# Kernel optimization log

Measured on AMD Instinct MI355X. Metric: run time of the kernel, lower is better.

## Reference

```python
import jax, jax.numpy as jnp
import numpy as np

B, T, C, H = 2, 2048, 1024, 16
HD = C // H  # head dim = 64


def setup_inputs() -> dict:
    key = jax.random.key(0)
    ks = jax.random.split(key, 5)
    s = 1.0 / np.sqrt(C)
    return {
        "x": jax.random.normal(ks[0], (B, T, C), dtype=jnp.float32),
        "W_attn": jax.random.normal(ks[1], (3 * C, C), dtype=jnp.float32) * s,
        "b_attn": jax.random.normal(ks[2], (3 * C,), dtype=jnp.float32) * 0.02,
        "W_proj": jax.random.normal(ks[3], (C, C), dtype=jnp.float32) * s,
        "b_proj": jax.random.normal(ks[4], (C,), dtype=jnp.float32) * 0.02,
    }


def reference(x, W_attn, b_attn, W_proj, b_proj):
    Bx, Tx, Cx = x.shape
    # fused QKV projection (torch Linear: x @ W.T + b)
    qkv = x @ W_attn.T + b_attn                      # [B,T,3C]
    q, k, v = jnp.split(qkv, 3, axis=-1)
    # [B,T,C] -> [B,H,T,hd]
    q = q.reshape(Bx, Tx, H, HD).transpose(0, 2, 1, 3)
    k = k.reshape(Bx, Tx, H, HD).transpose(0, 2, 1, 3)
    v = v.reshape(Bx, Tx, H, HD).transpose(0, 2, 1, 3)
    scale = 1.0 / np.sqrt(HD)
    att = jnp.einsum('bhqd,bhkd->bhqk', q, k) * scale  # [B,H,T,T]
    causal = jnp.tril(jnp.ones((Tx, Tx), dtype=bool))
    att = jnp.where(causal[None, None], att, -jnp.inf)
    att = jax.nn.softmax(att, axis=-1)
    y = jnp.einsum('bhqk,bhkd->bhqd', att, v)          # [B,H,T,hd]
    y = y.transpose(0, 2, 1, 3).reshape(Bx, Tx, Cx)
    return y @ W_proj.T + b_proj
```

## Files before the change

kernel.cpp:

```cpp
#include <hip/hip_runtime.h>

typedef unsigned short ushort_t;
typedef __bf16 bf16x8 __attribute__((ext_vector_type(8)));
typedef float f32x4 __attribute__((ext_vector_type(4)));
typedef unsigned u32x4 __attribute__((ext_vector_type(4)));

__device__ inline ushort_t f2bf(float f) {
  unsigned int u = __builtin_bit_cast(unsigned int, f);
  u += 0x7fff + ((u >> 16) & 1);
  return (ushort_t)(u >> 16);
}

__device__ inline unsigned pk_bf(float a, float b) {
  unsigned r;
  asm("v_cvt_pk_bf16_f32 %0, %1, %2" : "=v"(r) : "v"(a), "v"(b));
  return r;
}

__device__ inline void async_ld16(const ushort_t* g, const ushort_t* l) {
  __builtin_amdgcn_global_load_lds(
      (const __attribute__((address_space(1))) void*)g,
      (__attribute__((address_space(3))) void*)l, 16, 0, 0);
}

template <int IMM>
__device__ inline void waitcnt_barrier() {
  asm volatile("" ::: "memory");
  __builtin_amdgcn_s_waitcnt(IMM);
  __builtin_amdgcn_s_barrier();
  asm volatile("" ::: "memory");
}

__global__ void cvt_all(const float* __restrict__ x, const float* __restrict__ wa,
                        const float* __restrict__ wp, ushort_t* __restrict__ xb,
                        ushort_t* __restrict__ wab, ushort_t* __restrict__ wpb) {
  int i = blockIdx.x * 256 + threadIdx.x;
  const float* src;
  ushort_t* dst;
  int off;
  if (i < 1048576) { src = x; dst = xb; off = i; }
  else if (i < 1835008) { src = wa; dst = wab; off = i - 1048576; }
  else { src = wp; dst = wpb; off = i - 1835008; }
  float4 f = ((const float4*)src)[off];
  unsigned long long p = (unsigned long long)f2bf(f.x)
      | ((unsigned long long)f2bf(f.y) << 16)
      | ((unsigned long long)f2bf(f.z) << 32)
      | ((unsigned long long)f2bf(f.w) << 48);
  ((unsigned long long*)dst)[off] = p;
}

template <int BM, int BN, int IM, int JN, int MODE, int TPB>
__global__ __launch_bounds__(TPB) void gemm_bt(
    const ushort_t* __restrict__ A, const ushort_t* __restrict__ B,
    const float* __restrict__ bias, float* __restrict__ Cf,
    ushort_t* __restrict__ Cb, ushort_t* __restrict__ vtb,
    int M, int N, int K, int ldc, float qscale) {
  constexpr int NWN = BN / (JN * 16);
  constexpr int NL = (BM + BN) * 32 / (TPB * 8);
  constexpr int WIMM = 0x0F70 | NL;
  __shared__ __align__(16) ushort_t As[3][BM * 32];
  __shared__ __align__(16) ushort_t Bs[3][BN * 32];
  const int tid = threadIdx.x;
  const int wave = tid >> 6, lane = tid & 63;
  const int quad = lane >> 4, l16 = lane & 15;
  const int wr = wave / NWN, wc = wave % NWN;
  const int wm = wr * IM * 16, wn = wc * JN * 16;
  const int m0 = blockIdx.y * BM, n0 = blockIdx.x * BN;
  const ushort_t* Ag = A + (size_t)m0 * K;
  const ushort_t* Bg = B + (size_t)n0 * K;
  const int slot = (quad ^ ((l16 >> 1) & 3)) * 8;
  f32x4 acc[IM][JN] = {};

  auto stage = [&](int kt, int bsel) {
    int k0 = kt * 32;
#pragma unroll
    for (int p = 0; p < BM * 4 / TPB; ++p) {
      int ci = p * TPB + tid;
      int row = ci >> 2, ch = (ci & 3) ^ ((ci >> 3) & 3);
      async_ld16(Ag + (size_t)row * K + k0 + ch * 8, As[bsel] + (p * TPB + wave * 64) * 8);
    }
#pragma unroll
    for (int p = 0; p < BN * 4 / TPB; ++p) {
      int ci = p * TPB + tid;
      int row = ci >> 2, ch = (ci & 3) ^ ((ci >> 3) & 3);
      async_ld16(Bg + (size_t)row * K + k0 + ch * 8, Bs[bsel] + (p * TPB + wave * 64) * 8);
    }
  };

  const int KT = K / 32;
  stage(0, 0);
  stage(1, 1);
  for (int kt = 0; kt < KT; ++kt) {
    waitcnt_barrier<WIMM>();
    if (kt + 2 < KT) stage(kt + 2, (kt + 2) % 3);
    const ushort_t* Ac = As[kt % 3];
    const ushort_t* Bc = Bs[kt % 3];
    bf16x8 af[IM], bfr[JN];
#pragma unroll
    for (int i = 0; i < IM; ++i)
      af[i] = *(const bf16x8*)(Ac + (wm + i * 16 + l16) * 32 + slot);
#pragma unroll
    for (int j = 0; j < JN; ++j)
      bfr[j] = *(const bf16x8*)(Bc + (wn + j * 16 + l16) * 32 + slot);
#pragma unroll
    for (int i = 0; i < IM; ++i)
#pragma unroll
      for (int j = 0; j < JN; ++j)
        acc[i][j] = __builtin_amdgcn_mfma_f32_16x16x32_bf16(af[i], bfr[j], acc[i][j], 0, 0, 0);
  }

  if (MODE == 1 && n0 >= 2048) {
#pragma unroll
    for (int j = 0; j < JN; ++j) {
      int col = n0 + wn + j * 16 + l16;
      int cv = col - 2048;
      float bv = bias[col];
      size_t rowbase = ((size_t)(cv >> 6)) * 64 + (cv & 63);
#pragma unroll
      for (int i = 0; i < IM; ++i) {
        int rowb = m0 + wm + i * 16 + quad * 4;
        int bb = rowb >> 11, t = rowb & 2047;
        uint2 pp;
        pp.x = pk_bf(acc[i][j][0] + bv, acc[i][j][1] + bv);
        pp.y = pk_bf(acc[i][j][2] + bv, acc[i][j][3] + bv);
        *(uint2*)(vtb + (((size_t)bb * 1024 + rowbase) * 2048 + t)) = pp;
      }
    }
    return;
  }
#pragma unroll
  for (int j = 0; j < JN; ++j) {
    int col = n0 + wn + j * 16 + l16;
    float bv = bias[col];
    float sc = (MODE == 1 && col < 1024) ? qscale : 1.0f;
#pragma unroll
    for (int i = 0; i < IM; ++i)
#pragma unroll
      for (int r = 0; r < 4; ++r) {
        int row = m0 + wm + i * 16 + quad * 4 + r;
        float v = (acc[i][j][r] + bv) * sc;
        if (MODE == 1)
          Cb[(size_t)row * ldc + col] = f2bf(v);
        else
          Cf[(size_t)row * ldc + col] = v;
      }
  }
}

__global__ __launch_bounds__(256, 2) void flash7(
    const ushort_t* __restrict__ qk, const ushort_t* __restrict__ vt,
    ushort_t* __restrict__ y) {
  __shared__ __align__(16) ushort_t Kb[3][4096];
  __shared__ __align__(16) ushort_t Vb[3][4096];
  const int tid = threadIdx.x, wave = tid >> 6, lane = tid & 63;
  const int quad = lane >> 4, l16 = lane & 15;
  const int r7 = l16 & 7;
  const int fK = (l16 & 3) | (((l16 >> 2) & 1) << 2);
  const int kbase = (16 * (l16 >> 2) + (l16 & 3)) * 64;
  const int xx = blockIdx.x, bh = blockIdx.y;
  const int Q = (bh < 16) ? (15 - xx) : xx;
  const int b = bh >> 4, h = bh & 15;
  const int bT = b * 2048;
  const int qw = Q * 128 + wave * 32;

  bf16x8 qf[2][2];
#pragma unroll
  for (int f = 0; f < 2; ++f) {
    const ushort_t* qrow = qk + (size_t)(bT + qw + f * 16 + l16) * 2048 + h * 64 + quad * 8;
    qf[f][0] = *(const bf16x8*)(qrow);
    qf[f][1] = *(const bf16x8*)(qrow + 32);
  }

  auto stage = [&](int kt, int bsel) {
    int k0 = kt * 64;
#pragma unroll
    for (int i = 0; i < 2; ++i) {
      int ci = i * 256 + tid;
      int row = ci >> 3;
      int chk = (ci & 7) ^ ((row & 3) | (((row >> 4) & 1) << 2));
      int chv = (ci & 7) ^ (row & 7);
      async_ld16(qk + (size_t)(bT + k0 + row) * 2048 + 1024 + h * 64 + chk * 8,
                 Kb[bsel] + (i * 256 + wave * 64) * 8);
      async_ld16(vt + (size_t)(bh * 64 + row) * 2048 + k0 + chv * 8,
                 Vb[bsel] + (i * 256 + wave * 64) * 8);
    }
  };

  f32x4 o[4][2] = {};
  float lac[2] = {0.f, 0.f};
  const int KT = 2 * Q + 2;

  stage(0, 0);
  stage(1, 1);
  for (int kt = 0; kt < KT; ++kt) {
    const int cur = kt % 3;
    if (kt + 1 < KT) waitcnt_barrier<0x0F74>();
    else             waitcnt_barrier<0x0F70>();
    if (kt + 2 < KT) stage(kt + 2, (kt + 2) % 3);
    const ushort_t* Kc = Kb[cur];
    const ushort_t* Vc = Vb[cur];
    bf16x8 kf[4][2];
#pragma unroll
    for (int j = 0; j < 4; ++j)
#pragma unroll
      for (int ks = 0; ks < 2; ++ks)
        kf[j][ks] = *(const bf16x8*)(Kc + kbase + j * 256 + (((ks * 4 + quad) ^ fK) * 8));
    f32x4 s[4][2] = {};
#pragma unroll
    for (int ks = 0; ks < 2; ++ks)
#pragma unroll
      for (int j = 0; j < 4; ++j) {
        s[j][0] = __builtin_amdgcn_mfma_f32_16x16x32_bf16(kf[j][ks], qf[0][ks], s[j][0], 0, 0, 0);
        s[j][1] = __builtin_amdgcn_mfma_f32_16x16x32_bf16(kf[j][ks], qf[1][ks], s[j][1], 0, 0, 0);
      }
    if (kt >= KT - 2) {
#pragma unroll
      for (int f = 0; f < 2; ++f) {
        int qloc = qw + f * 16 + l16;
#pragma unroll
        for (int j = 0; j < 4; ++j)
#pragma unroll
          for (int r = 0; r < 4; ++r)
            if (kt * 64 + quad * 16 + j * 4 + r > qloc) s[j][f][r] = -1e30f;
      }
    }
#pragma unroll
    for (int f = 0; f < 2; ++f)
#pragma unroll
      for (int j = 0; j < 4; ++j)
#pragma unroll
        for (int r = 0; r < 4; ++r) {
          float pv = exp2f(s[j][f][r]);
          s[j][f][r] = pv;
          lac[f] += pv;
        }
    bf16x8 pf[2][2];
#pragma unroll
    for (int ks = 0; ks < 2; ++ks)
#pragma unroll
      for (int f = 0; f < 2; ++f) {
        u32x4 w;
        w[0] = pk_bf(s[2 * ks][f][0], s[2 * ks][f][1]);
        w[1] = pk_bf(s[2 * ks][f][2], s[2 * ks][f][3]);
        w[2] = pk_bf(s[2 * ks + 1][f][0], s[2 * ks + 1][f][1]);
        w[3] = pk_bf(s[2 * ks + 1][f][2], s[2 * ks + 1][f][3]);
        pf[ks][f] = __builtin_bit_cast(bf16x8, w);
      }
#pragma unroll
    for (int ks = 0; ks < 2; ++ks)
#pragma unroll
      for (int j = 0; j < 4; ++j) {
        bf16x8 vf = *(const bf16x8*)(Vc + (j * 16 + l16) * 64 + (((ks + 2 * quad) ^ r7) * 8));
        o[j][0] = __builtin_amdgcn_mfma_f32_16x16x32_bf16(vf, pf[ks][0], o[j][0], 0, 0, 0);
        o[j][1] = __builtin_amdgcn_mfma_f32_16x16x32_bf16(vf, pf[ks][1], o[j][1], 0, 0, 0);
      }
  }

#pragma unroll
  for (int f = 0; f < 2; ++f) {
    float l = lac[f];
    l += __shfl_xor(l, 16, 64);
    l += __shfl_xor(l, 32, 64);
    float inv = 1.f / l;
    size_t row = (size_t)(bT + qw + f * 16 + l16);
#pragma unroll
    for (int j = 0; j < 4; ++j) {
      uint2 pp;
      pp.x = pk_bf(o[j][f][0] * inv, o[j][f][1] * inv);
      pp.y = pk_bf(o[j][f][2] * inv, o[j][f][3] * inv);
      *(uint2*)(y + row * 1024 + h * 64 + j * 16 + quad * 4) = pp;
    }
  }
}

extern "C" void kernel_launch(void* const* d_in, const int* in_sizes, int n_in,
                              void* d_out, int out_size, void* d_ws, size_t ws_size,
                              hipStream_t stream) {
  const float* x  = (const float*)d_in[0];
  const float* Wa = (const float*)d_in[1];
  const float* ba = (const float*)d_in[2];
  const float* Wp = (const float*)d_in[3];
  const float* bp = (const float*)d_in[4];
  float* out = (float*)d_out;
  char* ws = (char*)d_ws;
  ushort_t* xb  = (ushort_t*)(ws);
  ushort_t* Wab = (ushort_t*)(ws + 8388608);
  ushort_t* Wpb = (ushort_t*)(ws + 14680064);
  ushort_t* qkb = (ushort_t*)(ws + 16777216);
  ushort_t* yb  = (ushort_t*)(ws + 33554432);
  ushort_t* vtb = (ushort_t*)(ws + 41943040);

  cvt_all<<<8192, 256, 0, stream>>>(x, Wa, Wp, xb, Wab, Wpb);
  gemm_bt<128, 128, 4, 2, 1, 512><<<dim3(24, 32), 512, 0, stream>>>(
      xb, Wab, ba, nullptr, qkb, vtb, 4096, 3072, 1024, 2048, 0.18033688011112042f);
  flash7<<<dim3(16, 32), 256, 0, stream>>>(qkb, vtb, yb);
  gemm_bt<64, 64, 2, 2, 0, 256><<<dim3(16, 64), 256, 0, stream>>>(
      yb, Wpb, bp, out, nullptr, nullptr, 4096, 1024, 1024, 1024, 1.0f);
}
```

Before: 188.8 us.

## Split flash attention block across 8 waves with 16 query rows each and 4-stage pipeline

The flash attention kernel now launches 512 threads per block (8 waves), each wave owning 16 query rows instead of 32, which halves per-wave register state for scores and outputs. Each thread issues one async load per tile instead of two, and the K/V LDS ring grows from 3 to 4 buffers with a prefetch distance of 3 tiles. The waitcnt is adjusted for the deeper pipeline. This trades higher LDS use (64KB per block) and more waves competing for LDS reads of K/V, since each K/V fragment now feeds only one query fragment, for more latency hiding and occupancy.

```diff
diff --git a/kernel.cpp b/kernel.cpp
--- a/kernel.cpp
+++ b/kernel.cpp
@@ -147,11 +147,11 @@
   }
 }
 
-__global__ __launch_bounds__(256, 2) void flash7(
+__global__ __launch_bounds__(512, 4) void flash8(
     const ushort_t* __restrict__ qk, const ushort_t* __restrict__ vt,
     ushort_t* __restrict__ y) {
-  __shared__ __align__(16) ushort_t Kb[3][4096];
-  __shared__ __align__(16) ushort_t Vb[3][4096];
+  __shared__ __align__(16) ushort_t Kb[4][4096];
+  __shared__ __align__(16) ushort_t Vb[4][4096];
   const int tid = threadIdx.x, wave = tid >> 6, lane = tid & 63;
   const int quad = lane >> 4, l16 = lane & 15;
   const int r7 = l16 & 7;
@@ -161,42 +161,40 @@
   const int Q = (bh < 16) ? (15 - xx) : xx;
   const int b = bh >> 4, h = bh & 15;
   const int bT = b * 2048;
-  const int qw = Q * 128 + wave * 32;
-
-  bf16x8 qf[2][2];
-#pragma unroll
-  for (int f = 0; f < 2; ++f) {
-    const ushort_t* qrow = qk + (size_t)(bT + qw + f * 16 + l16) * 2048 + h * 64 + quad * 8;
-    qf[f][0] = *(const bf16x8*)(qrow);
-    qf[f][1] = *(const bf16x8*)(qrow + 32);
+  const int qw = Q * 128 + wave * 16;
+
+  bf16x8 qf[2];
+  {
+    const ushort_t* qrow = qk + (size_t)(bT + qw + l16) * 2048 + h * 64 + quad * 8;
+    qf[0] = *(const bf16x8*)(qrow);
+    qf[1] = *(const bf16x8*)(qrow + 32);
   }
 
   auto stage = [&](int kt, int bsel) {
     int k0 = kt * 64;
-#pragma unroll
-    for (int i = 0; i < 2; ++i) {
-      int ci = i * 256 + tid;
-      int row = ci >> 3;
-      int chk = (ci & 7) ^ ((row & 3) | (((row >> 4) & 1) << 2));
-      int chv = (ci & 7) ^ (row & 7);
-      async_ld16(qk + (size_t)(bT + k0 + row) * 2048 + 1024 + h * 64 + chk * 8,
-                 Kb[bsel] + (i * 256 + wave * 64) * 8);
-      async_ld16(vt + (size_t)(bh * 64 + row) * 2048 + k0 + chv * 8,
-                 Vb[bsel] + (i * 256 + wave * 64) * 8);
-    }
+    int row = tid >> 3;
+    int chk = (tid & 7) ^ ((row & 3) | (((row >> 4) & 1) << 2));
+    int chv = (tid & 7) ^ (row & 7);
+    async_ld16(qk + (size_t)(bT + k0 + row) * 2048 + 1024 + h * 64 + chk * 8,
+               Kb[bsel] + wave * 512);
+    async_ld16(vt + (size_t)(bh * 64 + row) * 2048 + k0 + chv * 8,
+               Vb[bsel] + wave * 512);
   };
 
-  f32x4 o[4][2] = {};
-  float lac[2] = {0.f, 0.f};
+  f32x4 o[4] = {};
+  float lac0 = 0.f, lac1 = 0.f;
   const int KT = 2 * Q + 2;
 
   stage(0, 0);
   stage(1, 1);
+  if (KT > 2) stage(2, 2);
   for (int kt = 0; kt < KT; ++kt) {
-    const int cur = kt % 3;
-    if (kt + 1 < KT) waitcnt_barrier<0x0F74>();
-    else             waitcnt_barrier<0x0F70>();
-    if (kt + 2 < KT) stage(kt + 2, (kt + 2) % 3);
+    const int cur = kt & 3;
+    int ahead = KT - 1 - kt;
+    if (ahead >= 2)      waitcnt_barrier<0x0F74>();
+    else if (ahead == 1) waitcnt_barrier<0x0F72>();
+    else                 waitcnt_barrier<0x0F70>();
+    if (kt + 3 < KT) stage(kt + 3, (kt + 3) & 3);
     const ushort_t* Kc = Kb[cur];
     const ushort_t* Vc = Vb[cur];
     bf16x8 kf[4][2];
@@ -205,69 +203,58 @@
 #pragma unroll
       for (int ks = 0; ks < 2; ++ks)
         kf[j][ks] = *(const bf16x8*)(Kc + kbase + j * 256 + (((ks * 4 + quad) ^ fK) * 8));
-    f32x4 s[4][2] = {};
+    f32x4 s[4] = {};
 #pragma unroll
     for (int ks = 0; ks < 2; ++ks)
 #pragma unroll
-      for (int j = 0; j < 4; ++j) {
-        s[j][0] = __builtin_amdgcn_mfma_f32_16x16x32_bf16(kf[j][ks], qf[0][ks], s[j][0], 0, 0, 0);
-        s[j][1] = __builtin_amdgcn_mfma_f32_16x16x32_bf16(kf[j][ks], qf[1][ks], s[j][1], 0, 0, 0);
-      }
+      for (int j = 0; j < 4; ++j)
+        s[j] = __builtin_amdgcn_mfma_f32_16x16x32_bf16(kf[j][ks], qf[ks], s[j], 0, 0, 0);
     if (kt >= KT - 2) {
-#pragma unroll
-      for (int f = 0; f < 2; ++f) {
-        int qloc = qw + f * 16 + l16;
-#pragma unroll
-        for (int j = 0; j < 4; ++j)
-#pragma unroll
-          for (int r = 0; r < 4; ++r)
-            if (kt * 64 + quad * 16 + j * 4 + r > qloc) s[j][f][r] = -1e30f;
-      }
-    }
-#pragma unroll
-    for (int f = 0; f < 2; ++f)
+      int qloc = qw + l16;
 #pragma unroll
       for (int j = 0; j < 4; ++j)
 #pragma unroll
-        for (int r = 0; r < 4; ++r) {
-          float pv = exp2f(s[j][f][r]);
-          s[j][f][r] = pv;
-          lac[f] += pv;
-        }
-    bf16x8 pf[2][2];
-#pragma unroll
-    for (int ks = 0; ks < 2; ++ks)
-#pragma unroll
-      for (int f = 0; f < 2; ++f) {
-        u32x4 w;
-        w[0] = pk_bf(s[2 * ks][f][0], s[2 * ks][f][1]);
-        w[1] = pk_bf(s[2 * ks][f][2], s[2 * ks][f][3]);
-        w[2] = pk_bf(s[2 * ks + 1][f][0], s[2 * ks + 1][f][1]);
-        w[3] = pk_bf(s[2 * ks + 1][f][2], s[2 * ks + 1][f][3]);
-        pf[ks][f] = __builtin_bit_cast(bf16x8, w);
-      }
+        for (int r = 0; r < 4; ++r)
+          if (kt * 64 + quad * 16 + j * 4 + r > qloc) s[j][r] = -1e30f;
+    }
+#pragma unroll
+    for (int j = 0; j < 4; ++j)
+#pragma unroll
+      for (int r = 0; r < 4; ++r) {
+        float pv = exp2f(s[j][r]);
+        s[j][r] = pv;
+        if (j & 1) lac1 += pv; else lac0 += pv;
+      }
+    bf16x8 pf[2];
+#pragma unroll
+    for (int ks = 0; ks < 2; ++ks) {
+      u32x4 w;
+      w[0] = pk_bf(s[2 * ks][0], s[2 * ks][1]);
+      w[1] = pk_bf(s[2 * ks][2], s[2 * ks][3]);
+      w[2] = pk_bf(s[2 * ks + 1][0], s[2 * ks + 1][1]);
+      w[3] = pk_bf(s[2 * ks + 1][2], s[2 * ks + 1][3]);
+      pf[ks] = __builtin_bit_cast(bf16x8, w);
+    }
 #pragma unroll
     for (int ks = 0; ks < 2; ++ks)
 #pragma unroll
       for (int j = 0; j < 4; ++j) {
         bf16x8 vf = *(const bf16x8*)(Vc + (j * 16 + l16) * 64 + (((ks + 2 * quad) ^ r7) * 8));
-        o[j][0] = __builtin_amdgcn_mfma_f32_16x16x32_bf16(vf, pf[ks][0], o[j][0], 0, 0, 0);
-        o[j][1] = __builtin_amdgcn_mfma_f32_16x16x32_bf16(vf, pf[ks][1], o[j][1], 0, 0, 0);
-      }
-  }
-
-#pragma unroll
-  for (int f = 0; f < 2; ++f) {
-    float l = lac[f];
+        o[j] = __builtin_amdgcn_mfma_f32_16x16x32_bf16(vf, pf[ks], o[j], 0, 0, 0);
+      }
+  }
+
+  {
+    float l = lac0 + lac1;
     l += __shfl_xor(l, 16, 64);
     l += __shfl_xor(l, 32, 64);
     float inv = 1.f / l;
-    size_t row = (size_t)(bT + qw + f * 16 + l16);
+    size_t row = (size_t)(bT + qw + l16);
 #pragma unroll
     for (int j = 0; j < 4; ++j) {
       uint2 pp;
-      pp.x = pk_bf(o[j][f][0] * inv, o[j][f][1] * inv);
-      pp.y = pk_bf(o[j][f][2] * inv, o[j][f][3] * inv);
+      pp.x = pk_bf(o[j][0] * inv, o[j][1] * inv);
+      pp.y = pk_bf(o[j][2] * inv, o[j][3] * inv);
       *(uint2*)(y + row * 1024 + h * 64 + j * 16 + quad * 4) = pp;
     }
   }
@@ -293,7 +280,7 @@
   cvt_all<<<8192, 256, 0, stream>>>(x, Wa, Wp, xb, Wab, Wpb);
   gemm_bt<128, 128, 4, 2, 1, 512><<<dim3(24, 32), 512, 0, stream>>>(
       xb, Wab, ba, nullptr, qkb, vtb, 4096, 3072, 1024, 2048, 0.18033688011112042f);
-  flash7<<<dim3(16, 32), 256, 0, stream>>>(qkb, vtb, yb);
+  flash8<<<dim3(16, 32), 512, 0, stream>>>(qkb, vtb, yb);
   gemm_bt<64, 64, 2, 2, 0, 256><<<dim3(16, 64), 256, 0, stream>>>(
       yb, Wpb, bp, out, nullptr, nullptr, 4096, 1024, 1024, 1024, 1.0f);
 }
```

After: 181.2 us. -4.1%, faster.
